# Optimization experiments

Measured on AMD Instinct MI355X. Metric: run time of the kernel, lower is better.

The kernel has to match this reference:

```python
import jax, jax.numpy as jnp
import numpy as np

H = 1024
M = 4096
K = 64            # max_memory_updates_per_step
THRESH = 0.5      # surprise_threshold
EPS = 1e-12


def setup_inputs() -> dict:
    key = jax.random.key(0)
    ks = jax.random.split(key, 5)
    B, S = 4, 2048
    return {
        "hidden_states": jax.random.normal(ks[0], (B, S, H), dtype=jnp.float32),
        "ln_gamma": jnp.ones((H,), jnp.float32),
        "ln_beta": jnp.zeros((H,), jnp.float32),
        "Wq": jax.random.normal(ks[1], (H, H), jnp.float32) * 0.02,
        "bq": jnp.zeros((H,), jnp.float32),
        "Wo": jax.random.normal(ks[2], (H, H), jnp.float32) * 0.02,
        "bo": jnp.zeros((H,), jnp.float32),
        "memory": jax.random.normal(ks[3], (M, H), jnp.float32),
        "importance_scores": jax.random.uniform(ks[4], (M,), jnp.float32),
    }


def _layer_norm(x, g, b):
    mu = jnp.mean(x, axis=-1, keepdims=True)
    var = jnp.mean(jnp.square(x - mu), axis=-1, keepdims=True)
    return (x - mu) * jax.lax.rsqrt(var + EPS) * g + b


def reference(hidden_states, ln_gamma, ln_beta, Wq, bq, Wo, bo, memory, importance_scores):
    # LayerNorm
    norm = _layer_norm(hidden_states, ln_gamma, ln_beta)  # [B,S,H]

    # Surprise measure (detached): mean |x| over hidden dim
    surprise = jnp.mean(jnp.abs(jax.lax.stop_gradient(norm)), axis=-1)  # [B,S]

    # --- surprise-based memory update (buffers; no gradient, training mode) ---
    flat_h = jax.lax.stop_gradient(norm).reshape(-1, H)   # [B*S, H]
    flat_s = surprise.reshape(-1)                          # [B*S]
    # top-K surprises, descending (matches where>thr -> sort desc -> take K)
    top_vals, top_idx = jax.lax.top_k(flat_s, K)
    valid = top_vals > THRESH                              # entries below threshold: no write
    # K slots with smallest importance, ascending importance order
    _, slots = jax.lax.top_k(-importance_scores, K)
    new_rows = flat_h[top_idx]                             # [K, H]
    old_rows = memory[slots]                               # [K, H]
    mem = memory.at[slots].set(jnp.where(valid[:, None], new_rows, old_rows))  # [M,H]

    # --- query memory ---
    q = jnp.einsum("bsh,oh->bso", norm, Wq) + bq           # query_proj
    sim = jnp.einsum("bsh,mh->bsm", q, mem)                # [B,S,M]
    attn = jax.nn.softmax(sim, axis=-1)
    retrieved = jnp.einsum("bsm,mh->bsh", attn, mem)       # [B,S,H]
    mem_out = jnp.einsum("bsh,oh->bso", retrieved, Wo) + bo  # output_proj

    # dropout in eval mode = identity; residual add
    return hidden_states + mem_out
```

## Files before the change

kernel.cpp:

```cpp
#include <hip/hip_runtime.h>

#define H 1024
#define MMEM 4096
#define NTOK 8192
#define KTOP 64
#define FTHRESH 0.5f

typedef _Float16 half8 __attribute__((ext_vector_type(8)));
typedef float vf4 __attribute__((ext_vector_type(4)));

__device__ __forceinline__ short f2h(float x){
  union { _Float16 h; short s; } u; u.h = (_Float16)x; return u.s;
}
__device__ __forceinline__ float h2f(short s){
  union { _Float16 h; short s; } u; u.s = s; return (float)u.h;
}
__device__ __forceinline__ unsigned fkey_of(float x){
  unsigned u = __float_as_uint(x);
  return (u & 0x80000000u) ? ~u : (u | 0x80000000u);
}
__device__ __forceinline__ float val_of(unsigned k){
  unsigned u = (k & 0x80000000u) ? (k & 0x7fffffffu) : ~k;
  return __uint_as_float(u);
}

__device__ __forceinline__ void gload_lds16(const short* g, short* l){
  __builtin_amdgcn_global_load_lds(
      (const __attribute__((address_space(1))) unsigned int*)g,
      (__attribute__((address_space(3))) unsigned int*)l, 16, 0, 0);
}

__global__ __launch_bounds__(256) void ln_kernel(
    const float* __restrict__ hs, const float* __restrict__ g, const float* __restrict__ be,
    short* __restrict__ n16, float* __restrict__ surprise)
{
  int row = blockIdx.x, tid = threadIdx.x;
  long base = (long)row * H;
  float4 x = ((const float4*)(hs + base))[tid];
  float s1 = x.x + x.y + x.z + x.w;
  float s2 = x.x*x.x + x.y*x.y + x.z*x.z + x.w*x.w;
  __shared__ float r1[4], r2[4], r3[4];
  int w = tid >> 6, lane = tid & 63;
  for (int o = 32; o; o >>= 1){ s1 += __shfl_down(s1, o); s2 += __shfl_down(s2, o); }
  if (lane == 0){ r1[w] = s1; r2[w] = s2; }
  __syncthreads();
  float S1 = r1[0]+r1[1]+r1[2]+r1[3];
  float S2 = r2[0]+r2[1]+r2[2]+r2[3];
  float mean = S1 * (1.0f/H);
  float var  = S2 * (1.0f/H) - mean*mean;
  float rinv = rsqrtf(var + 1e-12f);
  float4 gg = ((const float4*)g)[tid];
  float4 bb = ((const float4*)be)[tid];
  float4 n;
  n.x = (x.x-mean)*rinv*gg.x + bb.x;
  n.y = (x.y-mean)*rinv*gg.y + bb.y;
  n.z = (x.z-mean)*rinv*gg.z + bb.z;
  n.w = (x.w-mean)*rinv*gg.w + bb.w;
  float sa = fabsf(n.x)+fabsf(n.y)+fabsf(n.z)+fabsf(n.w);
  for (int o = 32; o; o >>= 1) sa += __shfl_down(sa, o);
  if (lane == 0) r3[w] = sa;
  __syncthreads();
  if (tid == 0) surprise[row] = (r3[0]+r3[1]+r3[2]+r3[3]) * (1.0f/H);
  short4 h4;
  h4.x = f2h(n.x); h4.y = f2h(n.y); h4.z = f2h(n.z); h4.w = f2h(n.w);
  ((short4*)(n16 + base))[tid] = h4;
}

__global__ __launch_bounds__(256) void topk_local(
    const float* __restrict__ surprise, const float* __restrict__ imp,
    unsigned long long* __restrict__ cand_s, unsigned long long* __restrict__ cand_i)
{
  __shared__ unsigned long long s[256];
  int b = blockIdx.x, tid = threadIdx.x;
  int maxmode = (b < 32);
  int gidx = maxmode ? (b*256 + tid) : ((b-32)*256 + tid);
  float x = maxmode ? surprise[gidx] : imp[gidx];
  unsigned k = fkey_of(x);
  if (!maxmode) k = ~k;
  s[tid] = ((unsigned long long)k << 32) | (unsigned)(8191 - gidx);
  __syncthreads();
  for (int kk = 2; kk <= 256; kk <<= 1)
    for (int j = kk >> 1; j > 0; j >>= 1){
      int i = tid, ixj = i ^ j;
      if (ixj > i){
        bool asc = ((i & kk) == 0);
        unsigned long long a = s[i], c = s[ixj];
        if ((a < c) == asc){ s[i] = c; s[ixj] = a; }
      }
      __syncthreads();
    }
  if (tid < 64){
    if (maxmode) cand_s[b*64 + tid] = s[tid];
    else         cand_i[(b-32)*64 + tid] = s[tid];
  }
}

__global__ __launch_bounds__(256) void topk_merge(
    const unsigned long long* __restrict__ cand_s, const unsigned long long* __restrict__ cand_i,
    float* __restrict__ top_vals, int* __restrict__ top_idx, int* __restrict__ slots)
{
  __shared__ unsigned long long s[2048];
  int tid = threadIdx.x;
  int N = (blockIdx.x == 0) ? 2048 : 1024;
  const unsigned long long* src = (blockIdx.x == 0) ? cand_s : cand_i;
  for (int i = tid; i < N; i += 256) s[i] = src[i];
  __syncthreads();
  for (int kk = 2; kk <= N; kk <<= 1)
    for (int j = kk >> 1; j > 0; j >>= 1){
      for (int i = tid; i < N; i += 256){
        int ixj = i ^ j;
        if (ixj > i){
          bool asc = ((i & kk) == 0);
          unsigned long long a = s[i], c = s[ixj];
          if ((a < c) == asc){ s[i] = c; s[ixj] = a; }
        }
      }
      __syncthreads();
    }
  if (tid < 64){
    unsigned long long p = s[tid];
    int gi = 8191 - (int)(p & 0xffffffffu);
    if (blockIdx.x == 0){
      top_vals[tid] = val_of((unsigned)(p >> 32));
      top_idx[tid] = gi;
    } else {
      slots[tid] = gi;
    }
  }
}

__global__ __launch_bounds__(256) void prep_all_kernel(
    const float* __restrict__ mem, const float* __restrict__ Wq, const float* __restrict__ Wo,
    short* __restrict__ m16, short* __restrict__ wqT, short* __restrict__ wo16)
{
  int b = blockIdx.x, tid = threadIdx.x;
  if (b < 4096){
    long i = (long)b * 256 + tid;
    float4 x = ((const float4*)mem)[i];
    short4 h;
    h.x = f2h(x.x); h.y = f2h(x.y); h.z = f2h(x.z); h.w = f2h(x.w);
    ((short4*)m16)[i] = h;
  } else if (b < 5120){
    long i = (long)(b - 4096) * 256 + tid;
    float4 x = ((const float4*)Wo)[i];
    short4 h;
    h.x = f2h(x.x); h.y = f2h(x.y); h.z = f2h(x.z); h.w = f2h(x.w);
    ((short4*)wo16)[i] = h;
  } else {
    __shared__ __align__(16) short t[64][66];
    int tb = b - 5120;
    int r0 = (tb >> 4) * 64, c0 = (tb & 15) * 64;
    #pragma unroll
    for (int k = 0; k < 4; ++k){
      int idx = k*256 + tid;
      int r = idx >> 4, c4 = (idx & 15) * 4;
      float4 x = *(const float4*)&Wq[(long)(r0+r)*H + c0 + c4];
      t[r][c4]   = f2h(x.x);
      t[r][c4+1] = f2h(x.y);
      t[r][c4+2] = f2h(x.z);
      t[r][c4+3] = f2h(x.w);
    }
    __syncthreads();
    #pragma unroll
    for (int k = 0; k < 4; ++k){
      int idx = k*256 + tid;
      int c = idx >> 4, r4 = (idx & 15) * 4;
      short4 h;
      h.x = t[r4][c]; h.y = t[r4+1][c]; h.z = t[r4+2][c]; h.w = t[r4+3][c];
      *(short4*)&wqT[(long)(c0+c)*H + r0 + r4] = h;
    }
  }
}

__global__ __launch_bounds__(256) void update_kernel(
    const float* __restrict__ top_vals, const int* __restrict__ top_idx, const int* __restrict__ slots,
    const float* __restrict__ hs, const float* __restrict__ g, const float* __restrict__ be,
    short* __restrict__ m16)
{
  int i = blockIdx.x;
  if (top_vals[i] <= FTHRESH) return;
  int s = slots[i], r = top_idx[i];
  int tid = threadIdx.x, w = tid >> 6, lane = tid & 63;
  long base = (long)r * H;
  float4 x = ((const float4*)(hs + base))[tid];
  float s1 = x.x + x.y + x.z + x.w;
  float s2 = x.x*x.x + x.y*x.y + x.z*x.z + x.w*x.w;
  __shared__ float r1[4], r2[4];
  for (int o = 32; o; o >>= 1){ s1 += __shfl_down(s1, o); s2 += __shfl_down(s2, o); }
  if (lane == 0){ r1[w] = s1; r2[w] = s2; }
  __syncthreads();
  float S1 = r1[0]+r1[1]+r1[2]+r1[3];
  float S2 = r2[0]+r2[1]+r2[2]+r2[3];
  float mean = S1 * (1.0f/H);
  float var  = S2 * (1.0f/H) - mean*mean;
  float rinv = rsqrtf(var + 1e-12f);
  float4 gg = ((const float4*)g)[tid];
  float4 bb = ((const float4*)be)[tid];
  short4 h4;
  h4.x = f2h((x.x-mean)*rinv*gg.x + bb.x);
  h4.y = f2h((x.y-mean)*rinv*gg.y + bb.y);
  h4.z = f2h((x.z-mean)*rinv*gg.z + bb.z);
  h4.w = f2h((x.w-mean)*rinv*gg.w + bb.w);
  ((short4*)(m16 + (long)s*H))[tid] = h4;
}

__global__ __launch_bounds__(256) void bias_kernel(
    const float* __restrict__ bq, const short* __restrict__ m16, float* __restrict__ biasM)
{
  int tid = threadIdx.x, w = tid >> 6, lane = tid & 63;
  int m = blockIdx.x*4 + w;
  const short* ph = m16 + (long)m*H;
  float s = 0.f;
  for (int j = 0; j < 16; ++j){
    int h = lane + j*64;
    s += bq[h] * h2f(ph[h]);
  }
  for (int o = 32; o; o >>= 1) s += __shfl_down(s, o);
  if (lane == 0) biasM[m] = s;
}

template<int SPLIT, int MODE>
__global__ __launch_bounds__(256) void gemm128(
    const short* __restrict__ A,
    const short* __restrict__ Bh, const short* __restrict__ Bl,
    int K, int N,
    short* __restrict__ O1,
    float* __restrict__ Of, const float* __restrict__ resid, const float* __restrict__ biasN)
{
  __shared__ short sA[128*64];
  __shared__ short sBh[128*64];
  __shared__ short sBl[SPLIT ? 128*64 : 64];
  int tid = threadIdx.x, w = tid >> 6, lane = tid & 63, ln = lane & 15, quad = lane >> 4;
  int wr = w >> 1, wc = w & 1;
  int nwgx = gridDim.x;
  int nwg  = nwgx * gridDim.y;
  int lin  = blockIdx.y * nwgx + blockIdx.x;
  int nl   = (lin & 7) * (nwg >> 3) + (lin >> 3);
  long m0 = (long)(nl / nwgx) * 128, n0 = (long)(nl % nwgx) * 128;
  long Kl = K;
  vf4 acc[4][4];
  #pragma unroll
  for (int i = 0; i < 4; ++i) for (int j = 0; j < 4; ++j) for (int r = 0; r < 4; ++r) acc[i][j][r] = 0.0f;

  for (long kk = 0; kk < Kl; kk += 64){
    #pragma unroll
    for (int j = 0; j < 4; ++j){
      int f = (w*4 + j)*64 + lane;
      int row = f >> 3, c8 = f & 7;
      long go = kk + (long)((c8 ^ (row & 7)) * 8);
      gload_lds16(A  + (m0+row)*Kl + go, sA  + (w*4+j)*512);
      gload_lds16(Bh + (n0+row)*Kl + go, sBh + (w*4+j)*512);
      if (SPLIT) gload_lds16(Bl + (n0+row)*Kl + go, sBl + (w*4+j)*512);
    }
    __syncthreads();
    #pragma unroll
    for (int ks = 0; ks < 64; ks += 32){
      int cbase = (ks >> 3) + quad;
      half8 bh[4], bl[4];
      #pragma unroll
      for (int j = 0; j < 4; ++j){
        int rb = wc*64 + j*16 + ln;
        int cb = cbase ^ (rb & 7);
        bh[j] = *(const half8*)&sBh[rb*64 + cb*8];
        if (SPLIT) bl[j] = *(const half8*)&sBl[rb*64 + cb*8];
      }
      #pragma unroll
      for (int i = 0; i < 4; ++i){
        int ra = wr*64 + i*16 + ln;
        int ca = cbase ^ (ra & 7);
        half8 a = *(const half8*)&sA[ra*64 + ca*8];
        #pragma unroll
        for (int j = 0; j < 4; ++j){
          acc[i][j] = __builtin_amdgcn_mfma_f32_16x16x32_f16(a, bh[j], acc[i][j], 0, 0, 0);
          if (SPLIT)
            acc[i][j] = __builtin_amdgcn_mfma_f32_16x16x32_f16(a, bl[j], acc[i][j], 0, 0, 0);
        }
      }
    }
    __syncthreads();
  }

  #pragma unroll
  for (int i = 0; i < 4; ++i){
    #pragma unroll
    for (int j = 0; j < 4; ++j){
      #pragma unroll
      for (int r = 0; r < 4; ++r){
        long row = m0 + wr*64 + i*16 + quad*4 + r;
        long col = n0 + wc*64 + j*16 + ln;
        float v = acc[i][j][r];
        if (MODE == 1){
          O1[row*(long)N + col] = f2h(v + biasN[col]);
        } else if (MODE == 2){
          O1[row*(long)N + col] = f2h(v);
        } else {
          Of[row*(long)N + col] = v + resid[row*(long)N + col] + biasN[col];
        }
      }
    }
  }
}

template<int MODE>
__global__ __launch_bounds__(512, 2) void gemm256(
    const short* __restrict__ A, const short* __restrict__ B,
    int K, int N,
    short* __restrict__ O1, float* __restrict__ Of,
    const float* __restrict__ resid, const float* __restrict__ biasN)
{
  extern __shared__ short lds[];
  int tid = threadIdx.x, w = tid >> 6, lane = tid & 63, ln = lane & 15, quad = lane >> 4;
  int wr = w >> 2, wc = w & 3;
  int nwgx = gridDim.x, nwg = nwgx * gridDim.y;
  int lin = blockIdx.y * nwgx + blockIdx.x;
  int nl  = (lin & 7) * (nwg >> 3) + (lin >> 3);
  long m0 = (long)(nl / nwgx) * 256, n0 = (long)(nl % nwgx) * 256;
  long Kl = K;
  int NT = K >> 6;

  auto STAGE = [&](const short* __restrict__ G, long rowbase, long kt, short* ldsbase){
    #pragma unroll
    for (int i = 0; i < 2; ++i){
      int f = i*512 + tid;
      int row = f >> 3, c8 = f & 7;
      long go = kt + (long)((c8 ^ (row & 7)) * 8);
      gload_lds16(G + (rowbase + row)*Kl + go, ldsbase + i*4096 + w*512);
    }
  };
  auto LOADA = [&](half8 (&af)[4][2], const short* sAh){
    #pragma unroll
    for (int ks = 0; ks < 2; ++ks){
      int cbase = ks*4 + quad;
      #pragma unroll
      for (int i = 0; i < 4; ++i){
        int ra = wr*64 + i*16 + ln;
        af[i][ks] = *(const half8*)&sAh[ra*64 + (cbase ^ (ra & 7))*8];
      }
    }
  };
  auto LOADB = [&](half8 (&bf)[2][2], const short* sBh){
    #pragma unroll
    for (int ks = 0; ks < 2; ++ks){
      int cbase = ks*4 + quad;
      #pragma unroll
      for (int j = 0; j < 2; ++j){
        int rb = wc*32 + j*16 + ln;
        bf[j][ks] = *(const half8*)&sBh[rb*64 + (cbase ^ (rb & 7))*8];
      }
    }
  };

  vf4 acc[4][4][2];
  #pragma unroll
  for (int p = 0; p < 4; ++p)
    for (int i = 0; i < 4; ++i)
      for (int j = 0; j < 2; ++j)
        for (int r = 0; r < 4; ++r) acc[p][i][j][r] = 0.0f;

  {
    int t1 = (NT > 1) ? 1 : 0;
    STAGE(A, m0 + 0,   0, lds + 0);
    STAGE(B, n0 + 0,   0, lds + 16384);
    STAGE(B, n0 + 128, 0, lds + 16384 + 8192);
    STAGE(A, m0 + 128, 0, lds + 8192);
    STAGE(A, m0 + 0,   (long)t1*64, lds + 32768);
    STAGE(B, n0 + 0,   (long)t1*64, lds + 32768 + 16384);
  }
  asm volatile("s_waitcnt vmcnt(8)" ::: "memory");
  asm volatile("s_barrier" ::: "memory");

  #define PH_PRE()  do { \
    asm volatile("s_barrier" ::: "memory"); \
    asm volatile("s_waitcnt lgkmcnt(0)" ::: "memory"); \
    __builtin_amdgcn_sched_barrier(0); \
    __builtin_amdgcn_s_setprio(1); } while(0)
  #define PH_POST() do { \
    __builtin_amdgcn_s_setprio(0); \
    asm volatile("s_waitcnt vmcnt(8)" ::: "memory"); \
    asm volatile("s_barrier" ::: "memory"); } while(0)
  #define MFMA16(ap, af, bf) do { \
    _Pragma("unroll") \
    for (int i = 0; i < 4; ++i){ \
      _Pragma("unroll") \
      for (int j = 0; j < 2; ++j){ \
        ap[i][j] = __builtin_amdgcn_mfma_f32_16x16x32_f16(af[i][0], bf[j][0], ap[i][j], 0, 0, 0); \
        ap[i][j] = __builtin_amdgcn_mfma_f32_16x16x32_f16(af[i][1], bf[j][1], ap[i][j], 0, 0, 0); \
      } \
    } } while(0)

  for (int t = 0; t < NT; ++t){
    int cur = t & 1;
    short* bA = lds + cur*32768;
    short* bB = bA + 16384;
    short* oA = lds + (cur^1)*32768;
    short* oB = oA + 16384;
    int t1 = t + 1; if (t1 >= NT) t1 -= NT;
    int t2 = t + 2; if (t2 >= NT) t2 -= NT;
    long kt1 = (long)t1 * 64, kt2 = (long)t2 * 64;
    half8 af[4][2], bf0[2][2], bf1[2][2];

    LOADA(af, bA);
    LOADB(bf0, bB);
    STAGE(B, n0 + 128, kt1, oB + 8192);
    PH_PRE();
    MFMA16(acc[0], af, bf0);
    PH_POST();

    LOADB(bf1, bB + 8192);
    STAGE(A, m0 + 128, kt1, oA + 8192);
    PH_PRE();
    MFMA16(acc[1], af, bf1);
    PH_POST();

    LOADA(af, bA + 8192);
    STAGE(A, m0 + 0, kt2, bA);
    PH_PRE();
    MFMA16(acc[2], af, bf0);
    PH_POST();

    STAGE(B, n0 + 0, kt2, bB);
    PH_PRE();
    MFMA16(acc[3], af, bf1);
    PH_POST();
  }
  #undef PH_PRE
  #undef PH_POST
  #undef MFMA16

  float bn[2][2];
  if (MODE != 2){
    #pragma unroll
    for (int bh = 0; bh < 2; ++bh)
      for (int j = 0; j < 2; ++j)
        bn[bh][j] = biasN[n0 + bh*128 + wc*32 + j*16 + ln];
  }
  #pragma unroll
  for (int p = 0; p < 4; ++p){
    #pragma unroll
    for (int i = 0; i < 4; ++i){
      #pragma unroll
      for (int j = 0; j < 2; ++j){
        #pragma unroll
        for (int r = 0; r < 4; ++r){
          long row = m0 + (p >> 1)*128 + wr*64 + i*16 + quad*4 + r;
          long col = n0 + (p & 1)*128 + wc*32 + j*16 + ln;
          float v = acc[p][i][j][r];
          if (MODE == 1){
            O1[row*(long)N + col] = f2h(v + bn[p & 1][j]);
          } else if (MODE == 2){
            O1[row*(long)N + col] = f2h(v);
          } else {
            Of[row*(long)N + col] = v + resid[row*(long)N + col] + bn[p & 1][j];
          }
        }
      }
    }
  }
}

__global__ __launch_bounds__(256) void softmax_kernel(short* __restrict__ simP)
{
  long row = blockIdx.x;
  int tid = threadIdx.x, w = tid >> 6, lane = tid & 63;
  half8* ptr = (half8*)(simP + row*MMEM);
  float xf[16];
  float mx = -1e30f;
  #pragma unroll
  for (int j = 0; j < 2; ++j){
    half8 x = ptr[tid + j*256];
    #pragma unroll
    for (int e = 0; e < 8; ++e){ float f = (float)x[e]; xf[j*8+e] = f; mx = fmaxf(mx, f); }
  }
  for (int o = 32; o; o >>= 1) mx = fmaxf(mx, __shfl_xor(mx, o));
  __shared__ float rmax[4], rsum[4];
  if (lane == 0) rmax[w] = mx;
  __syncthreads();
  mx = fmaxf(fmaxf(rmax[0], rmax[1]), fmaxf(rmax[2], rmax[3]));
  float p[16], s = 0.f;
  #pragma unroll
  for (int k = 0; k < 16; ++k){ p[k] = __expf(xf[k] - mx); s += p[k]; }
  for (int o = 32; o; o >>= 1) s += __shfl_xor(s, o);
  if (lane == 0) rsum[w] = s;
  __syncthreads();
  float inv = 1.0f / (rsum[0]+rsum[1]+rsum[2]+rsum[3]);
  #pragma unroll
  for (int j = 0; j < 2; ++j){
    half8 o8;
    #pragma unroll
    for (int e = 0; e < 8; ++e) o8[e] = (_Float16)(p[j*8+e] * inv);
    ptr[tid + j*256] = o8;
  }
}

extern "C" void kernel_launch(void* const* d_in, const int* in_sizes, int n_in,
                              void* d_out, int out_size, void* d_ws, size_t ws_size,
                              hipStream_t stream)
{
  const float* hs  = (const float*)d_in[0];
  const float* gam = (const float*)d_in[1];
  const float* bet = (const float*)d_in[2];
  const float* Wq  = (const float*)d_in[3];
  const float* bq  = (const float*)d_in[4];
  const float* Wo  = (const float*)d_in[5];
  const float* bo  = (const float*)d_in[6];
  const float* mem = (const float*)d_in[7];
  const float* imp = (const float*)d_in[8];
  float* out = (float*)d_out;

  char* ws = (char*)d_ws;
  short* n16   = (short*)(ws);
  short* g16   = (short*)(ws + (16ull<<20));
  short* m16   = (short*)(ws + (32ull<<20));
  short* wqT   = (short*)(ws + (40ull<<20));
  short* simP  = (short*)(ws + (48ull<<20));
  short* vwoT  = (short*)(ws + (112ull<<20));
  short* wo16  = (short*)(ws + (132ull<<20));
  char*  tail  = ws + (134ull<<20);
  float* biasM    = (float*)tail;
  float* surprise = (float*)(tail + (64<<10));
  float* top_vals = (float*)(tail + (128<<10));
  int*   top_idx  = (int*)  (tail + (129<<10));
  int*   slots    = (int*)  (tail + (130<<10));
  unsigned long long* cand_s = (unsigned long long*)(tail + (132<<10));
  unsigned long long* cand_i = (unsigned long long*)(tail + (148<<10));

  static bool attr_done = false;
  if (!attr_done){
    (void)hipFuncSetAttribute(reinterpret_cast<const void*>(&gemm256<1>),
                              hipFuncAttributeMaxDynamicSharedMemorySize, 131072);
    attr_done = true;
  }

  ln_kernel<<<NTOK, 256, 0, stream>>>(hs, gam, bet, n16, surprise);
  topk_local<<<48, 256, 0, stream>>>(surprise, imp, cand_s, cand_i);
  topk_merge<<<2, 256, 0, stream>>>(cand_s, cand_i, top_vals, top_idx, slots);
  prep_all_kernel<<<5376, 256, 0, stream>>>(mem, Wq, Wo, m16, wqT, wo16);
  update_kernel<<<KTOP, 256, 0, stream>>>(top_vals, top_idx, slots, hs, gam, bet, m16);
  bias_kernel<<<1024, 256, 0, stream>>>(bq, m16, biasM);
  gemm128<0,2><<<dim3(32,8), 256, 0, stream>>>(
      wo16, m16, m16, H, MMEM, vwoT, nullptr, nullptr, nullptr);
  gemm128<0,2><<<dim3(8,32), 256, 0, stream>>>(
      m16, wqT, wqT, H, H, g16, nullptr, nullptr, nullptr);
  gemm256<1><<<dim3(16,32), 512, 131072, stream>>>(
      n16, g16, H, MMEM, simP, nullptr, nullptr, biasM);
  softmax_kernel<<<NTOK, 256, 0, stream>>>(simP);
  gemm128<0,3><<<dim3(8,64), 256, 0, stream>>>(
      simP, vwoT, vwoT, MMEM, H, nullptr, out, hs, bo);
}
```

Before: 407.3 us.

## Fuse bias into prep/update, merge small GEMMs, add pipelined output GEMM

Folds the bias_kernel row dot-products into prep_all_kernel and update_kernel, so the separate bias pass is gone. The two precompute GEMMs (Wo·mem and mem·WqT) are merged into one launch of 512 workgroups. The final attn·vwoT GEMM (K=4096) moves from a 128x128 tile kernel to a new 128x256 tile kernel with 512 threads and double-buffered LDS staging at 96 KB. That kernel interleaves loads with MFMA phases using barriers and priority hints. These changes cut launch count and improve overlap and reuse on the largest-K GEMM, at the cost of more complex synchronisation.

```diff
diff --git a/kernel.cpp b/kernel.cpp
--- a/kernel.cpp
+++ b/kernel.cpp
@@ -131,7 +131,9 @@
 
 __global__ __launch_bounds__(256) void prep_all_kernel(
     const float* __restrict__ mem, const float* __restrict__ Wq, const float* __restrict__ Wo,
-    short* __restrict__ m16, short* __restrict__ wqT, short* __restrict__ wo16)
+    const float* __restrict__ bq,
+    short* __restrict__ m16, short* __restrict__ wqT, short* __restrict__ wo16,
+    float* __restrict__ biasM)
 {
   int b = blockIdx.x, tid = threadIdx.x;
   if (b < 4096){
@@ -140,6 +142,14 @@
     short4 h;
     h.x = f2h(x.x); h.y = f2h(x.y); h.z = f2h(x.z); h.w = f2h(x.w);
     ((short4*)m16)[i] = h;
+    float4 b4 = ((const float4*)bq)[tid];
+    float sb = b4.x*h2f(h.x) + b4.y*h2f(h.y) + b4.z*h2f(h.z) + b4.w*h2f(h.w);
+    int wv = tid >> 6, lane = tid & 63;
+    for (int o = 32; o; o >>= 1) sb += __shfl_down(sb, o);
+    __shared__ float rb_[4];
+    if (lane == 0) rb_[wv] = sb;
+    __syncthreads();
+    if (tid == 0) biasM[b] = rb_[0]+rb_[1]+rb_[2]+rb_[3];
   } else if (b < 5120){
     long i = (long)(b - 4096) * 256 + tid;
     float4 x = ((const float4*)Wo)[i];
@@ -175,7 +185,8 @@
 __global__ __launch_bounds__(256) void update_kernel(
     const float* __restrict__ top_vals, const int* __restrict__ top_idx, const int* __restrict__ slots,
     const float* __restrict__ hs, const float* __restrict__ g, const float* __restrict__ be,
-    short* __restrict__ m16)
+    const float* __restrict__ bq,
+    short* __restrict__ m16, float* __restrict__ biasM)
 {
   int i = blockIdx.x;
   if (top_vals[i] <= FTHRESH) return;
@@ -185,7 +196,7 @@
   float4 x = ((const float4*)(hs + base))[tid];
   float s1 = x.x + x.y + x.z + x.w;
   float s2 = x.x*x.x + x.y*x.y + x.z*x.z + x.w*x.w;
-  __shared__ float r1[4], r2[4];
+  __shared__ float r1[4], r2[4], rb[4];
   for (int o = 32; o; o >>= 1){ s1 += __shfl_down(s1, o); s2 += __shfl_down(s2, o); }
   if (lane == 0){ r1[w] = s1; r2[w] = s2; }
   __syncthreads();
@@ -202,41 +213,33 @@
   h4.z = f2h((x.z-mean)*rinv*gg.z + bb.z);
   h4.w = f2h((x.w-mean)*rinv*gg.w + bb.w);
   ((short4*)(m16 + (long)s*H))[tid] = h4;
-}
-
-__global__ __launch_bounds__(256) void bias_kernel(
-    const float* __restrict__ bq, const short* __restrict__ m16, float* __restrict__ biasM)
-{
-  int tid = threadIdx.x, w = tid >> 6, lane = tid & 63;
-  int m = blockIdx.x*4 + w;
-  const short* ph = m16 + (long)m*H;
-  float s = 0.f;
-  for (int j = 0; j < 16; ++j){
-    int h = lane + j*64;
-    s += bq[h] * h2f(ph[h]);
-  }
-  for (int o = 32; o; o >>= 1) s += __shfl_down(s, o);
-  if (lane == 0) biasM[m] = s;
-}
-
-template<int SPLIT, int MODE>
-__global__ __launch_bounds__(256) void gemm128(
-    const short* __restrict__ A,
-    const short* __restrict__ Bh, const short* __restrict__ Bl,
-    int K, int N,
-    short* __restrict__ O1,
-    float* __restrict__ Of, const float* __restrict__ resid, const float* __restrict__ biasN)
+  float4 b4 = ((const float4*)bq)[tid];
+  float sb = b4.x*h2f(h4.x) + b4.y*h2f(h4.y) + b4.z*h2f(h4.z) + b4.w*h2f(h4.w);
+  for (int o = 32; o; o >>= 1) sb += __shfl_down(sb, o);
+  if (lane == 0) rb[w] = sb;
+  __syncthreads();
+  if (tid == 0) biasM[s] = rb[0]+rb[1]+rb[2]+rb[3];
+}
+
+__global__ __launch_bounds__(256) void gemm_dual(
+    const short* __restrict__ A0, const short* __restrict__ B0, int N0, short* __restrict__ O0,
+    const short* __restrict__ A1, const short* __restrict__ B1, int N1, short* __restrict__ O1,
+    int K)
 {
   __shared__ short sA[128*64];
-  __shared__ short sBh[128*64];
-  __shared__ short sBl[SPLIT ? 128*64 : 64];
+  __shared__ short sB[128*64];
   int tid = threadIdx.x, w = tid >> 6, lane = tid & 63, ln = lane & 15, quad = lane >> 4;
   int wr = w >> 1, wc = w & 1;
-  int nwgx = gridDim.x;
-  int nwg  = nwgx * gridDim.y;
-  int lin  = blockIdx.y * nwgx + blockIdx.x;
-  int nl   = (lin & 7) * (nwg >> 3) + (lin >> 3);
-  long m0 = (long)(nl / nwgx) * 128, n0 = (long)(nl % nwgx) * 128;
+  int lin = blockIdx.x;
+  int nl  = (lin & 7) * 64 + (lin >> 3);
+  int second = (nl >= 256);
+  int t = second ? (nl - 256) : nl;
+  const short* A = second ? A1 : A0;
+  const short* B = second ? B1 : B0;
+  short* O = second ? O1 : O0;
+  int N = second ? N1 : N0;
+  int nwgx = N >> 7;
+  long m0 = (long)(t / nwgx) * 128, n0 = (long)(t % nwgx) * 128;
   long Kl = K;
   vf4 acc[4][4];
   #pragma unroll
@@ -248,57 +251,41 @@
       int f = (w*4 + j)*64 + lane;
       int row = f >> 3, c8 = f & 7;
       long go = kk + (long)((c8 ^ (row & 7)) * 8);
-      gload_lds16(A  + (m0+row)*Kl + go, sA  + (w*4+j)*512);
-      gload_lds16(Bh + (n0+row)*Kl + go, sBh + (w*4+j)*512);
-      if (SPLIT) gload_lds16(Bl + (n0+row)*Kl + go, sBl + (w*4+j)*512);
+      gload_lds16(A + (m0+row)*Kl + go, sA + (w*4+j)*512);
+      gload_lds16(B + (n0+row)*Kl + go, sB + (w*4+j)*512);
     }
     __syncthreads();
     #pragma unroll
     for (int ks = 0; ks < 64; ks += 32){
       int cbase = (ks >> 3) + quad;
-      half8 bh[4], bl[4];
+      half8 bh[4];
       #pragma unroll
       for (int j = 0; j < 4; ++j){
         int rb = wc*64 + j*16 + ln;
-        int cb = cbase ^ (rb & 7);
-        bh[j] = *(const half8*)&sBh[rb*64 + cb*8];
-        if (SPLIT) bl[j] = *(const half8*)&sBl[rb*64 + cb*8];
+        bh[j] = *(const half8*)&sB[rb*64 + (cbase ^ (rb & 7))*8];
       }
       #pragma unroll
       for (int i = 0; i < 4; ++i){
         int ra = wr*64 + i*16 + ln;
-        int ca = cbase ^ (ra & 7);
-        half8 a = *(const half8*)&sA[ra*64 + ca*8];
+        half8 a = *(const half8*)&sA[ra*64 + (cbase ^ (ra & 7))*8];
         #pragma unroll
-        for (int j = 0; j < 4; ++j){
+        for (int j = 0; j < 4; ++j)
           acc[i][j] = __builtin_amdgcn_mfma_f32_16x16x32_f16(a, bh[j], acc[i][j], 0, 0, 0);
-          if (SPLIT)
-            acc[i][j] = __builtin_amdgcn_mfma_f32_16x16x32_f16(a, bl[j], acc[i][j], 0, 0, 0);
-        }
       }
     }
     __syncthreads();
   }
 
   #pragma unroll
-  for (int i = 0; i < 4; ++i){
-    #pragma unroll
-    for (int j = 0; j < 4; ++j){
+  for (int i = 0; i < 4; ++i)
+    #pragma unroll
+    for (int j = 0; j < 4; ++j)
       #pragma unroll
       for (int r = 0; r < 4; ++r){
         long row = m0 + wr*64 + i*16 + quad*4 + r;
         long col = n0 + wc*64 + j*16 + ln;
-        float v = acc[i][j][r];
-        if (MODE == 1){
-          O1[row*(long)N + col] = f2h(v + biasN[col]);
-        } else if (MODE == 2){
-          O1[row*(long)N + col] = f2h(v);
-        } else {
-          Of[row*(long)N + col] = v + resid[row*(long)N + col] + biasN[col];
-        }
-      }
-    }
-  }
+        O[row*(long)N + col] = f2h(acc[i][j][r]);
+      }
 }
 
 template<int MODE>
@@ -458,6 +445,157 @@
   }
 }
 
+__global__ __launch_bounds__(512, 2) void gemm_out(
+    const short* __restrict__ A, const short* __restrict__ B,
+    int K, int N,
+    float* __restrict__ Of, const float* __restrict__ resid, const float* __restrict__ biasN)
+{
+  extern __shared__ short lds[];
+  int tid = threadIdx.x, w = tid >> 6, lane = tid & 63, ln = lane & 15, quad = lane >> 4;
+  int wr = (w >> 2) & 1, wc = w & 3;
+  int nwgx = gridDim.x, nwg = nwgx * gridDim.y;
+  int lin = blockIdx.y * nwgx + blockIdx.x;
+  int nl  = (lin & 7) * (nwg >> 3) + (lin >> 3);
+  int mtiles = gridDim.y;
+  long m0 = (long)(nl % mtiles) * 128, n0 = (long)(nl / mtiles) * 256;
+  long Kl = K;
+  int NT = K >> 6;
+
+  auto STAGE_A = [&](long rowbase, long kt, short* dst){
+    int f = tid;
+    int row = f >> 3, c8 = f & 7;
+    long go = kt + (long)((c8 ^ (row & 7)) * 8);
+    gload_lds16(A + (rowbase + row)*Kl + go, dst + w*512);
+  };
+  auto STAGE_B = [&](long rowbase, long kt, short* dst){
+    #pragma unroll
+    for (int i = 0; i < 2; ++i){
+      int f = i*512 + tid;
+      int row = f >> 3, c8 = f & 7;
+      long go = kt + (long)((c8 ^ (row & 7)) * 8);
+      gload_lds16(B + (rowbase + row)*Kl + go, dst + i*4096 + w*512);
+    }
+  };
+  auto LOADA = [&](half8 (&af)[2][2], const short* sAh){
+    #pragma unroll
+    for (int ks = 0; ks < 2; ++ks){
+      int cbase = ks*4 + quad;
+      #pragma unroll
+      for (int i = 0; i < 2; ++i){
+        int ra = wr*32 + i*16 + ln;
+        af[i][ks] = *(const half8*)&sAh[ra*64 + (cbase ^ (ra & 7))*8];
+      }
+    }
+  };
+  auto LOADB = [&](half8 (&bf)[2][2], const short* sBh){
+    #pragma unroll
+    for (int ks = 0; ks < 2; ++ks){
+      int cbase = ks*4 + quad;
+      #pragma unroll
+      for (int j = 0; j < 2; ++j){
+        int rb = wc*32 + j*16 + ln;
+        bf[j][ks] = *(const half8*)&sBh[rb*64 + (cbase ^ (rb & 7))*8];
+      }
+    }
+  };
+
+  vf4 acc[4][2][2];
+  #pragma unroll
+  for (int p = 0; p < 4; ++p)
+    for (int i = 0; i < 2; ++i)
+      for (int j = 0; j < 2; ++j)
+        for (int r = 0; r < 4; ++r) acc[p][i][j][r] = 0.0f;
+
+  {
+    int t1 = (NT > 1) ? 1 : 0;
+    STAGE_A(m0 + 0,   0, lds + 0);
+    STAGE_B(n0 + 0,   0, lds + 8192);
+    STAGE_B(n0 + 128, 0, lds + 16384);
+    STAGE_A(m0 + 64,  0, lds + 4096);
+    STAGE_A(m0 + 0,   (long)t1*64, lds + 24576);
+    STAGE_B(n0 + 0,   (long)t1*64, lds + 24576+8192);
+  }
+  asm volatile("s_waitcnt vmcnt(6)" ::: "memory");
+  asm volatile("s_barrier" ::: "memory");
+
+  #define FPH_PRE()  do { \
+    asm volatile("s_barrier" ::: "memory"); \
+    asm volatile("s_waitcnt lgkmcnt(0)" ::: "memory"); \
+    __builtin_amdgcn_sched_barrier(0); \
+    __builtin_amdgcn_s_setprio(1); } while(0)
+  #define FPH_POST() do { \
+    __builtin_amdgcn_s_setprio(0); \
+    asm volatile("s_waitcnt vmcnt(6)" ::: "memory"); \
+    asm volatile("s_barrier" ::: "memory"); } while(0)
+  #define MFMA8(ap, af, bf) do { \
+    _Pragma("unroll") \
+    for (int i = 0; i < 2; ++i){ \
+      _Pragma("unroll") \
+      for (int j = 0; j < 2; ++j){ \
+        ap[i][j] = __builtin_amdgcn_mfma_f32_16x16x32_f16(af[i][0], bf[j][0], ap[i][j], 0, 0, 0); \
+        ap[i][j] = __builtin_amdgcn_mfma_f32_16x16x32_f16(af[i][1], bf[j][1], ap[i][j], 0, 0, 0); \
+      } \
+    } } while(0)
+
+  for (int t = 0; t < NT; ++t){
+    int cur = t & 1;
+    short* bA = lds + cur*24576;
+    short* oA = lds + (cur^1)*24576;
+    int t1 = t + 1; if (t1 >= NT) t1 -= NT;
+    int t2 = t + 2; if (t2 >= NT) t2 -= NT;
+    long kt1 = (long)t1 * 64, kt2 = (long)t2 * 64;
+    half8 af[2][2], bf0[2][2], bf1[2][2];
+
+    LOADA(af, bA);
+    LOADB(bf0, bA + 8192);
+    STAGE_B(n0 + 128, kt1, oA + 16384);
+    FPH_PRE();
+    MFMA8(acc[0], af, bf0);
+    FPH_POST();
+
+    LOADB(bf1, bA + 16384);
+    STAGE_A(m0 + 64, kt1, oA + 4096);
+    FPH_PRE();
+    MFMA8(acc[1], af, bf1);
+    FPH_POST();
+
+    LOADA(af, bA + 4096);
+    STAGE_A(m0 + 0, kt2, bA);
+    FPH_PRE();
+    MFMA8(acc[2], af, bf0);
+    FPH_POST();
+
+    STAGE_B(n0 + 0, kt2, bA + 8192);
+    FPH_PRE();
+    MFMA8(acc[3], af, bf1);
+    FPH_POST();
+  }
+  #undef FPH_PRE
+  #undef FPH_POST
+  #undef MFMA8
+
+  float bn[2][2];
+  #pragma unroll
+  for (int bh = 0; bh < 2; ++bh)
+    for (int j = 0; j < 2; ++j)
+      bn[bh][j] = biasN[n0 + bh*128 + wc*32 + j*16 + ln];
+  #pragma unroll
+  for (int p = 0; p < 4; ++p){
+    #pragma unroll
+    for (int i = 0; i < 2; ++i){
+      #pragma unroll
+      for (int j = 0; j < 2; ++j){
+        #pragma unroll
+        for (int r = 0; r < 4; ++r){
+          long row = m0 + (p >> 1)*64 + wr*32 + i*16 + quad*4 + r;
+          long col = n0 + (p & 1)*128 + wc*32 + j*16 + ln;
+          Of[row*(long)N + col] = acc[p][i][j][r] + resid[row*(long)N + col] + bn[p & 1][j];
+        }
+      }
+    }
+  }
+}
+
 __global__ __launch_bounds__(256) void softmax_kernel(short* __restrict__ simP)
 {
   long row = blockIdx.x;
@@ -528,22 +666,21 @@
   if (!attr_done){
     (void)hipFuncSetAttribute(reinterpret_cast<const void*>(&gemm256<1>),
                               hipFuncAttributeMaxDynamicSharedMemorySize, 131072);
+    (void)hipFuncSetAttribute(reinterpret_cast<const void*>(&gemm_out),
+                              hipFuncAttributeMaxDynamicSharedMemorySize, 98304);
     attr_done = true;
   }
 
   ln_kernel<<<NTOK, 256, 0, stream>>>(hs, gam, bet, n16, surprise);
   topk_local<<<48, 256, 0, stream>>>(surprise, imp, cand_s, cand_i);
   topk_merge<<<2, 256, 0, stream>>>(cand_s, cand_i, top_vals, top_idx, slots);
-  prep_all_kernel<<<5376, 256, 0, stream>>>(mem, Wq, Wo, m16, wqT, wo16);
-  update_kernel<<<KTOP, 256, 0, stream>>>(top_vals, top_idx, slots, hs, gam, bet, m16);
-  bias_kernel<<<1024, 256, 0, stream>>>(bq, m16, biasM);
-  gemm128<0,2><<<dim3(32,8), 256, 0, stream>>>(
-      wo16, m16, m16, H, MMEM, vwoT, nullptr, nullptr, nullptr);
-  gemm128<0,2><<<dim3(8,32), 256, 0, stream>>>(
-      m16, wqT, wqT, H, H, g16, nullptr, nullptr, nullptr);
+  prep_all_kernel<<<5376, 256, 0, stream>>>(mem, Wq, Wo, bq, m16, wqT, wo16, biasM);
+  update_kernel<<<KTOP, 256, 0, stream>>>(top_vals, top_idx, slots, hs, gam, bet, bq, m16, biasM);
+  gemm_dual<<<512, 256, 0, stream>>>(
+      wo16, m16, MMEM, vwoT,  m16, wqT, H, g16,  H);
   gemm256<1><<<dim3(16,32), 512, 131072, stream>>>(
       n16, g16, H, MMEM, simP, nullptr, nullptr, biasM);
   softmax_kernel<<<NTOK, 256, 0, stream>>>(simP);
-  gemm128<0,3><<<dim3(8,64), 256, 0, stream>>>(
-      simP, vwoT, vwoT, MMEM, H, nullptr, out, hs, bo);
-}
+  gemm_out<<<dim3(4, 64), 512, 98304, stream>>>(
+      simP, vwoT, MMEM, H, out, hs, bo);
+}
```

Result: faster. 376.0 us (-7.7%).
